# Optimization experiments

Hardware: AMD Instinct MI355X
Metric: run time of the kernel (lower is better)

The kernel has to match this reference:

```python
import jax, jax.numpy as jnp
import numpy as np

N = 100000   # nodes
E = 1200000  # edges
H = 64       # hidden_channels
G = 256      # graphs in the batch
C_IN = 1
C_OUT = 2


def setup_inputs() -> dict:
    key = jax.random.key(0)
    ks = jax.random.split(key, 16)

    def lin_w(k, fan_in, fan_out):
        bound = 1.0 / np.sqrt(fan_in)
        return jax.random.uniform(k, (fan_in, fan_out), jnp.float32, -bound, bound)

    def lin_b(k, fan_in, fan_out):
        bound = 1.0 / np.sqrt(fan_in)
        return jax.random.uniform(k, (fan_out,), jnp.float32, -bound, bound)

    return {
        "x": jax.random.normal(ks[0], (N, C_IN), jnp.float32),
        "edge_index": jax.random.randint(ks[1], (2, E), 0, N),
        "batch": jnp.sort(jax.random.randint(ks[2], (N,), 0, G)),
        "edge_weight": jax.random.uniform(ks[3], (E,), jnp.float32),
        # GraphConv 1: lin_rel (bias) + lin_root (no bias)
        "W1_rel": lin_w(ks[4], C_IN, H), "b1": lin_b(ks[5], C_IN, H), "W1_root": lin_w(ks[6], C_IN, H),
        # GraphConv 2
        "W2_rel": lin_w(ks[7], H, H), "b2": lin_b(ks[8], H, H), "W2_root": lin_w(ks[9], H, H),
        # GraphConv 3
        "W3_rel": lin_w(ks[10], H, H), "b3": lin_b(ks[11], H, H), "W3_root": lin_w(ks[12], H, H),
        # head
        "W_lin": lin_w(ks[13], H, C_OUT), "b_lin": lin_b(ks[14], H, C_OUT),
    }


def _graph_conv(x, src, dst, ew, W_rel, b_rel, W_root):
    # message: edge_weight * x[src]; aggr='add' to dst; then lin_rel(aggr) + lin_root(x)
    m = x[src] * ew[:, None]                                    # [E, C]
    agg = jax.ops.segment_sum(m, dst, num_segments=x.shape[0])  # [N, C]
    return agg @ W_rel + b_rel + x @ W_root


def reference(x, edge_index, batch, edge_weight,
              W1_rel, b1, W1_root, W2_rel, b2, W2_root, W3_rel, b3, W3_root,
              W_lin, b_lin):
    src, dst = edge_index[0], edge_index[1]
    h = jax.nn.relu(_graph_conv(x, src, dst, edge_weight, W1_rel, b1, W1_root))
    h = jax.nn.relu(_graph_conv(h, src, dst, edge_weight, W2_rel, b2, W2_root))
    h = _graph_conv(h, src, dst, edge_weight, W3_rel, b3, W3_root)
    # global mean pool over graph id
    sums = jax.ops.segment_sum(h, batch, num_segments=G)                        # [G, H]
    cnts = jax.ops.segment_sum(jnp.ones((h.shape[0],), h.dtype), batch, num_segments=G)
    pooled = sums / jnp.maximum(cnts, 1.0)[:, None]
    # dropout is identity in eval mode
    return pooled @ W_lin + b_lin                                               # [G, 2]
```

## Files before the change

### kernel.cpp

```cpp
#include <hip/hip_runtime.h>


#define BKT_SHIFT 7
#define BKT_SZ    128
#define NBK_MAX   1024
#define CHUNK     4096

static __device__ __forceinline__ float4 ld4(const float* p) {
    return *reinterpret_cast<const float4*>(p);
}
static __device__ __forceinline__ float rdlane(float v, int i) {
    return __int_as_float(__builtin_amdgcn_readlane(__float_as_int(v), i));
}

__global__ void k_small(const float* __restrict__ W3_rel, const float* __restrict__ b3,
                        const float* __restrict__ W3_root, const float* __restrict__ W_lin,
                        float4* __restrict__ MC4, float* __restrict__ b3W,
                        int* __restrict__ zbase, int zwords)
{
    int gt = blockIdx.x * 256 + threadIdx.x;
    for (int i = gt; i < zwords; i += gridDim.x * 256) zbase[i] = 0;

    if (blockIdx.x == 0) {
        int t = threadIdx.x;
        if (t < 64) {
            float sr0 = 0.f, sr1 = 0.f, so0 = 0.f, so1 = 0.f;
            for (int k = 0; k < 64; ++k) {
                float wl0 = W_lin[k * 2 + 0], wl1 = W_lin[k * 2 + 1];
                sr0 += W3_rel[t * 64 + k] * wl0;
                sr1 += W3_rel[t * 64 + k] * wl1;
                so0 += W3_root[t * 64 + k] * wl0;
                so1 += W3_root[t * 64 + k] * wl1;
            }
            MC4[t] = make_float4(sr0, sr1, so0, so1);
        }
        if (t < 2) {
            float s = 0.f;
            for (int k = 0; k < 64; ++k) s += b3[k] * W_lin[k * 2 + t];
            b3W[t] = s;
        }
    }
}

__global__ __launch_bounds__(256) void k_hist2(const int* __restrict__ dst,
                                               int* __restrict__ bcnt, int E, int NBK)
{
    __shared__ int lh[NBK_MAX];
    for (int i = threadIdx.x; i < NBK; i += 256) lh[i] = 0;
    __syncthreads();
    int e0 = blockIdx.x * CHUNK;
#pragma unroll
    for (int k = 0; k < 16; ++k) {
        int e = e0 + k * 256 + threadIdx.x;
        if (e < E) atomicAdd(&lh[dst[e] >> BKT_SHIFT], 1);
    }
    __syncthreads();
    for (int i = threadIdx.x; i < NBK; i += 256) {
        int v = lh[i];
        if (v) atomicAdd(&bcnt[i], v);
    }
}

__global__ __launch_bounds__(256) void k_scanb(const int* __restrict__ bcnt,
                                               int* __restrict__ bb, int NBK)
{
    __shared__ int tmp[256];
    int t = threadIdx.x;
    int loc[4]; int s = 0;
#pragma unroll
    for (int u = 0; u < 4; ++u) {
        int idx = t * 4 + u;
        loc[u] = (idx < NBK) ? bcnt[idx] : 0;
        s += loc[u];
    }
    tmp[t] = s;
    __syncthreads();
    for (int off = 1; off < 256; off <<= 1) {
        int v = (t >= off) ? tmp[t - off] : 0;
        __syncthreads();
        tmp[t] += v;
        __syncthreads();
    }
    int run = tmp[t] - s;
#pragma unroll
    for (int u = 0; u < 4; ++u) {
        int idx = t * 4 + u;
        if (idx < NBK) bb[idx] = run;
        run += loc[u];
    }
    if (t == 255) bb[NBK] = run;
}

__global__ __launch_bounds__(256) void k_scatter2(const int* __restrict__ src,
                                                  const int* __restrict__ dst,
                                                  const float* __restrict__ ew,
                                                  const int* __restrict__ bb,
                                                  int* __restrict__ cursor,
                                                  int2* __restrict__ ebuf, int E, int NBK)
{
    __shared__ int lofs[NBK_MAX + 1];
    __shared__ int rcur[NBK_MAX];
    __shared__ int delta[NBK_MAX];
    __shared__ int2 stage[CHUNK];
    __shared__ unsigned short sbkt[CHUNK];
    __shared__ int tmp[256];

    const int t = threadIdx.x;
    const int e0 = blockIdx.x * CHUNK;
    const int cnt = min(CHUNK, E - e0);

    for (int i = t; i < NBK; i += 256) lofs[i] = 0;
    __syncthreads();

    int   myb[16];
    int   mypk[16];
    float myw[16];
#pragma unroll
    for (int k = 0; k < 16; ++k) {
        int e = e0 + k * 256 + t;
        myb[k] = -1;
        if (e < E) {
            int d = dst[e];
            int b = d >> BKT_SHIFT;
            myb[k]  = b;
            mypk[k] = ((d & (BKT_SZ - 1)) << 17) | src[e];
            myw[k]  = ew[e];
            atomicAdd(&lofs[b], 1);
        }
    }
    __syncthreads();

    int loc[4]; int s = 0;
#pragma unroll
    for (int u = 0; u < 4; ++u) {
        int idx = t * 4 + u;
        loc[u] = (idx < NBK) ? lofs[idx] : 0;
        s += loc[u];
    }
    tmp[t] = s;
    __syncthreads();
    for (int off = 1; off < 256; off <<= 1) {
        int v = (t >= off) ? tmp[t - off] : 0;
        __syncthreads();
        tmp[t] += v;
        __syncthreads();
    }
    int run = tmp[t] - s;
#pragma unroll
    for (int u = 0; u < 4; ++u) {
        int idx = t * 4 + u;
        if (idx < NBK) { lofs[idx] = run; rcur[idx] = run; }
        run += loc[u];
    }
    if (t == 255) lofs[NBK] = run;
    __syncthreads();

    for (int b = t; b < NBK; b += 256) {
        int c = lofs[b + 1] - lofs[b];
        if (c > 0) {
            int g0 = atomicAdd(&cursor[b], c);
            delta[b] = bb[b] + g0 - lofs[b];
        }
    }
    __syncthreads();

#pragma unroll
    for (int k = 0; k < 16; ++k) {
        if (myb[k] >= 0) {
            int p = atomicAdd(&rcur[myb[k]], 1);
            stage[p] = make_int2(mypk[k], __float_as_int(myw[k]));
            sbkt[p]  = (unsigned short)myb[k];
        }
    }
    __syncthreads();

    for (int i = t; i < cnt; i += 256) {
        int b = sbkt[i];
        ebuf[delta[b] + i] = stage[i];
    }
}

__global__ __launch_bounds__(256) void k_sort3(const int2* __restrict__ ebuf,
                                               const int* __restrict__ bb,
                                               int* __restrict__ rowptr,
                                               int2* __restrict__ csr,
                                               int N, int E, int NBK)
{
    __shared__ int cnt_[BKT_SZ];
    __shared__ int sc[BKT_SZ];
    __shared__ int base_[BKT_SZ];
    __shared__ int cur_[BKT_SZ];

    const int t = threadIdx.x;
    const int bk = blockIdx.x;
    if (t < BKT_SZ) cnt_[t] = 0;
    __syncthreads();

    const int beg = bb[bk], end = bb[bk + 1];
    for (int i = beg + t; i < end; i += 256) {
        int dl = ebuf[i].x >> 17;
        atomicAdd(&cnt_[dl], 1);
    }
    __syncthreads();

    if (t < BKT_SZ) sc[t] = cnt_[t];
    __syncthreads();
    for (int off = 1; off < BKT_SZ; off <<= 1) {
        int v = (t < BKT_SZ && t >= off) ? sc[t - off] : 0;
        __syncthreads();
        if (t < BKT_SZ) sc[t] += v;
        __syncthreads();
    }
    if (t < BKT_SZ) {
        base_[t] = sc[t] - cnt_[t];
        cur_[t] = 0;
        int n = bk * BKT_SZ + t;
        if (n < N) rowptr[n] = beg + base_[t];
    }
    if (bk == 0 && t == 0) rowptr[N] = E;
    __syncthreads();

    for (int i = beg + t; i < end; i += 256) {
        int2 pw = ebuf[i];
        int dl = pw.x >> 17;
        int pos = beg + base_[dl] + atomicAdd(&cur_[dl], 1);
        csr[pos] = make_int2(pw.x & 0x1FFFF, pw.y);
    }
}

__global__ __launch_bounds__(256) void k_agg1(const int2* __restrict__ csr,
                                              const int* __restrict__ rowptr,
                                              const float* __restrict__ x,
                                              float2* __restrict__ axn, int N)
{
    int gt = blockIdx.x * 256 + threadIdx.x;
    int n = gt >> 2, p = gt & 3;
    if (n >= N) return;
    int b = rowptr[n], en = rowptr[n + 1];
    float a = 0.f;
    for (int e = b + p; e < en; e += 4) {
        int2 sw = csr[e];
        a = fmaf(__int_as_float(sw.y), x[sw.x], a);
    }
    a += __shfl_xor(a, 1);
    a += __shfl_xor(a, 2);
    if (p == 0) axn[n] = make_float2(a, x[n]);
}

__global__ __launch_bounds__(256) void k_agg2(const int2* __restrict__ csr,
                                              const int* __restrict__ rowptr,
                                              const float2* __restrict__ axn,
                                              const float* __restrict__ W1_rel,
                                              const float* __restrict__ b1,
                                              const float* __restrict__ W1_root,
                                              float* __restrict__ agg2, int N)
{
    int n = (blockIdx.x * 256 + threadIdx.x) >> 6;
    int lane = threadIdx.x & 63;
    if (n >= N) return;
    float wrel = W1_rel[lane], wroot = W1_root[lane], bj = b1[lane];
    int b = rowptr[n], en = rowptr[n + 1];
    float acc = 0.f;

    for (int base = b; base < en; base += 64) {
        int e = base + lane;
        float wv = 0.f;
        float2 ax = make_float2(0.f, 0.f);
        if (e < en) {
            int2 sw = csr[e];
            wv = __int_as_float(sw.y);
            ax = axn[sw.x];
        }
        int cnt = min(en - base, 64);
        int i = 0;
        for (; i + 4 <= cnt; i += 4) {
#pragma unroll
            for (int u = 0; u < 4; ++u) {
                float wi = rdlane(wv, i + u);
                float ai = rdlane(ax.x, i + u);
                float xi = rdlane(ax.y, i + u);
                float h = fmaxf(fmaf(ai, wrel, fmaf(xi, wroot, bj)), 0.f);
                acc = fmaf(wi, h, acc);
            }
        }
        for (; i < cnt; ++i) {
            float wi = rdlane(wv, i);
            float ai = rdlane(ax.x, i);
            float xi = rdlane(ax.y, i);
            float h = fmaxf(fmaf(ai, wrel, fmaf(xi, wroot, bj)), 0.f);
            acc = fmaf(wi, h, acc);
        }
    }
    agg2[(size_t)n * 64 + lane] = acc;
}

__global__ __launch_bounds__(256) void k_node2(const float* __restrict__ agg2,
                                               const float2* __restrict__ axn,
                                               const float* __restrict__ W2_rel,
                                               const float* __restrict__ W2_root,
                                               const float* __restrict__ b2,
                                               const float* __restrict__ W1_rel,
                                               const float* __restrict__ b1,
                                               const float* __restrict__ W1_root,
                                               const float* __restrict__ MCf,
                                               float2* __restrict__ z01,
                                               float2* __restrict__ z23, int N)
{
    __shared__ float As[128 * 65];

    const int t = threadIdx.x;
    const int n0 = blockIdx.x * 128;

#pragma unroll
    for (int it = 0; it < 8; ++it) {
        int idx = it * 256 + t;
        int nl = idx >> 4, q4 = (idx & 15) << 2;
        int n = n0 + nl;
        float4 a = (n < N) ? ld4(&agg2[(size_t)n * 64 + q4])
                           : make_float4(0.f, 0.f, 0.f, 0.f);
        float* row = &As[nl * 65 + q4];
        row[0] = a.x; row[1] = a.y; row[2] = a.z; row[3] = a.w;
    }
    __syncthreads();

    const int lane = t & 63;
    const int g = (t >> 7) & 1;
    const int hs = __builtin_amdgcn_readfirstlane((t >> 6) & 1);
    const int nl = g * 64 + lane;
    const int n = n0 + nl;
    float2 ax = (n < N) ? axn[n] : make_float2(0.f, 0.f);

    float4 acc[8];
#pragma unroll
    for (int q = 0; q < 8; ++q) acc[q] = make_float4(0.f, 0.f, 0.f, 0.f);

    const float* Asr = &As[nl * 65];

    for (int c = 0; c < 8; ++c) {
        float a_[8];
#pragma unroll
        for (int i = 0; i < 8; ++i) a_[i] = Asr[c * 8 + i];
#pragma unroll
        for (int i = 0; i < 8; ++i) {
            const float* wr = &W2_rel[(size_t)(c * 8 + i) * 64 + hs * 32];
#pragma unroll
            for (int q = 0; q < 8; ++q) {
                float4 w = ld4(wr + q * 4);
                acc[q].x = fmaf(a_[i], w.x, acc[q].x);
                acc[q].y = fmaf(a_[i], w.y, acc[q].y);
                acc[q].z = fmaf(a_[i], w.z, acc[q].z);
                acc[q].w = fmaf(a_[i], w.w, acc[q].w);
            }
        }
    }

    for (int c = 0; c < 8; ++c) {
        int k0 = c * 8;
        float4 w1ra = ld4(&W1_rel[k0]),  w1rb = ld4(&W1_rel[k0 + 4]);
        float4 w1oa = ld4(&W1_root[k0]), w1ob = ld4(&W1_root[k0 + 4]);
        float4 b1a  = ld4(&b1[k0]),      b1b  = ld4(&b1[k0 + 4]);
        float hk[8];
        hk[0] = fmaxf(fmaf(ax.x, w1ra.x, fmaf(ax.y, w1oa.x, b1a.x)), 0.f);
        hk[1] = fmaxf(fmaf(ax.x, w1ra.y, fmaf(ax.y, w1oa.y, b1a.y)), 0.f);
        hk[2] = fmaxf(fmaf(ax.x, w1ra.z, fmaf(ax.y, w1oa.z, b1a.z)), 0.f);
        hk[3] = fmaxf(fmaf(ax.x, w1ra.w, fmaf(ax.y, w1oa.w, b1a.w)), 0.f);
        hk[4] = fmaxf(fmaf(ax.x, w1rb.x, fmaf(ax.y, w1ob.x, b1b.x)), 0.f);
        hk[5] = fmaxf(fmaf(ax.x, w1rb.y, fmaf(ax.y, w1ob.y, b1b.y)), 0.f);
        hk[6] = fmaxf(fmaf(ax.x, w1rb.z, fmaf(ax.y, w1ob.z, b1b.z)), 0.f);
        hk[7] = fmaxf(fmaf(ax.x, w1rb.w, fmaf(ax.y, w1ob.w, b1b.w)), 0.f);
#pragma unroll
        for (int i = 0; i < 8; ++i) {
            const float* wo = &W2_root[(size_t)(k0 + i) * 64 + hs * 32];
#pragma unroll
            for (int q = 0; q < 8; ++q) {
                float4 w = ld4(wo + q * 4);
                acc[q].x = fmaf(hk[i], w.x, acc[q].x);
                acc[q].y = fmaf(hk[i], w.y, acc[q].y);
                acc[q].z = fmaf(hk[i], w.z, acc[q].z);
                acc[q].w = fmaf(hk[i], w.w, acc[q].w);
            }
        }
    }

    float z0 = 0.f, z1 = 0.f, z2 = 0.f, z3 = 0.f;
    const float* b2h = &b2[hs * 32];
#pragma unroll
    for (int q = 0; q < 8; ++q) {
        float4 bq = ld4(b2h + q * 4);
        int jb = hs * 32 + q * 4;
        float h2;
        h2 = fmaxf(acc[q].x + bq.x, 0.f);
        { const float* m = &MCf[(jb + 0) * 4];
          z0 = fmaf(h2, m[0], z0); z1 = fmaf(h2, m[1], z1);
          z2 = fmaf(h2, m[2], z2); z3 = fmaf(h2, m[3], z3); }
        h2 = fmaxf(acc[q].y + bq.y, 0.f);
        { const float* m = &MCf[(jb + 1) * 4];
          z0 = fmaf(h2, m[0], z0); z1 = fmaf(h2, m[1], z1);
          z2 = fmaf(h2, m[2], z2); z3 = fmaf(h2, m[3], z3); }
        h2 = fmaxf(acc[q].z + bq.z, 0.f);
        { const float* m = &MCf[(jb + 2) * 4];
          z0 = fmaf(h2, m[0], z0); z1 = fmaf(h2, m[1], z1);
          z2 = fmaf(h2, m[2], z2); z3 = fmaf(h2, m[3], z3); }
        h2 = fmaxf(acc[q].w + bq.w, 0.f);
        { const float* m = &MCf[(jb + 3) * 4];
          z0 = fmaf(h2, m[0], z0); z1 = fmaf(h2, m[1], z1);
          z2 = fmaf(h2, m[2], z2); z3 = fmaf(h2, m[3], z3); }
    }

    __syncthreads();
    float* zs = As;
    *reinterpret_cast<float4*>(&zs[(nl * 2 + hs) * 4]) = make_float4(z0, z1, z2, z3);
    __syncthreads();
    if (hs == 0 && n < N) {
        float4 p0 = *reinterpret_cast<float4*>(&zs[(nl * 2 + 0) * 4]);
        float4 p1 = *reinterpret_cast<float4*>(&zs[(nl * 2 + 1) * 4]);
        z01[n] = make_float2(p0.x + p1.x, p0.y + p1.y);
        z23[n] = make_float2(p0.z + p1.z, p0.w + p1.w);
    }
}

__global__ __launch_bounds__(256) void k_pool(const int2* __restrict__ csr,
                                              const int* __restrict__ rowptr,
                                              const int* __restrict__ batch,
                                              const float2* __restrict__ z01,
                                              const float2* __restrict__ z23,
                                              float* __restrict__ gacc, int N, int G)
{
    extern __shared__ float lds[];
    for (int i = threadIdx.x; i < 5 * G; i += 256) lds[i] = 0.f;
    __syncthreads();

    int gt = blockIdx.x * 256 + threadIdx.x;
    int n = gt >> 2, p = gt & 3;
    if (n < N) {
        int b = rowptr[n], en = rowptr[n + 1];
        float s0 = 0.f, s1 = 0.f;
        for (int e = b + p; e < en; e += 4) {
            int2 sw = csr[e];
            float w = __int_as_float(sw.y);
            float2 zz = z01[sw.x];
            s0 = fmaf(w, zz.x, s0);
            s1 = fmaf(w, zz.y, s1);
        }
        s0 += __shfl_xor(s0, 1);
        s0 += __shfl_xor(s0, 2);
        s1 += __shfl_xor(s1, 1);
        s1 += __shfl_xor(s1, 2);
        if (p == 0) {
            int bg = batch[n];
            float2 zw = z23[n];
            atomicAdd(&lds[bg * 5 + 0], s0);
            atomicAdd(&lds[bg * 5 + 1], s1);
            atomicAdd(&lds[bg * 5 + 2], zw.x);
            atomicAdd(&lds[bg * 5 + 3], zw.y);
            atomicAdd(&lds[bg * 5 + 4], 1.0f);
        }
    }
    __syncthreads();
    for (int i = threadIdx.x; i < 5 * G; i += 256) {
        float v = lds[i];
        if (v != 0.f) atomicAdd(&gacc[i], v);
    }
}

__global__ void k_final(const float* __restrict__ gacc, const float* __restrict__ b3W,
                        const float* __restrict__ b_lin, float* __restrict__ out, int G)
{
    int t = blockIdx.x * blockDim.x + threadIdx.x;
    if (t < G * 2) {
        int g = t >> 1, c = t & 1;
        float cnt = gacc[g * 5 + 4];
        float s = gacc[g * 5 + c] + gacc[g * 5 + 2 + c] + cnt * b3W[c];
        out[t] = s / fmaxf(cnt, 1.f) + b_lin[c];
    }
}

extern "C" void kernel_launch(void* const* d_in, const int* in_sizes, int n_in,
                              void* d_out, int out_size, void* d_ws, size_t ws_size,
                              hipStream_t stream)
{
    const float* x       = (const float*)d_in[0];
    const int*   ei      = (const int*)  d_in[1];
    const int*   batch   = (const int*)  d_in[2];
    const float* ew      = (const float*)d_in[3];
    const float* W1_rel  = (const float*)d_in[4];
    const float* b1      = (const float*)d_in[5];
    const float* W1_root = (const float*)d_in[6];
    const float* W2_rel  = (const float*)d_in[7];
    const float* b2      = (const float*)d_in[8];
    const float* W2_root = (const float*)d_in[9];
    const float* W3_rel  = (const float*)d_in[10];
    const float* b3      = (const float*)d_in[11];
    const float* W3_root = (const float*)d_in[12];
    const float* W_lin   = (const float*)d_in[13];
    const float* b_lin   = (const float*)d_in[14];
    float* out = (float*)d_out;

    const int N = in_sizes[0];
    const int E = in_sizes[3];
    const int G = out_size / 2;
    const int NBK = (N + BKT_SZ - 1) >> BKT_SHIFT;
    const int EB  = (E + CHUNK - 1) / CHUNK;
    const int* src = ei;
    const int* dst = ei + E;

    char* wsb = (char*)d_ws;
    size_t o = 0;
    auto take = [&](size_t bytes) -> char* {
        char* p = wsb + o;
        o += (bytes + 15) & ~(size_t)15;
        return p;
    };
    int*    cursor = (int*)   take((size_t)NBK * 4);
    int*    bcnt   = (int*)   take((size_t)NBK * 4);
    float*  gacc   = (float*) take((size_t)G * 5 * 4);
    size_t  zero_bytes = o;
    int*    bb     = (int*)   take((size_t)(NBK + 1) * 4);
    int*    rowptr = (int*)   take((size_t)(N + 1) * 4);
    int2*   ebuf   = (int2*)  take((size_t)E * 8);
    int2*   csr    = (int2*)  take((size_t)E * 8);
    float2* axn    = (float2*)take((size_t)N * 8);
    float*  agg2   = (float*) take((size_t)N * 64 * 4);
    float2* z01    = (float2*)take((size_t)N * 8);
    float2* z23    = (float2*)take((size_t)N * 8);
    float4* MC4    = (float4*)take(64 * 16);
    float*  b3W    = (float*) take(4 * 4);

    const int zwords = (int)(zero_bytes / 4);

    hipLaunchKernelGGL(k_small, dim3(8), dim3(256), 0, stream,
                       W3_rel, b3, W3_root, W_lin, MC4, b3W,
                       (int*)d_ws, zwords);

    hipLaunchKernelGGL(k_hist2, dim3(EB), dim3(256), 0, stream, dst, bcnt, E, NBK);
    hipLaunchKernelGGL(k_scanb, dim3(1), dim3(256), 0, stream, bcnt, bb, NBK);
    hipLaunchKernelGGL(k_scatter2, dim3(EB), dim3(256), 0, stream,
                       src, dst, ew, bb, cursor, ebuf, E, NBK);
    hipLaunchKernelGGL(k_sort3, dim3(NBK), dim3(256), 0, stream,
                       ebuf, bb, rowptr, csr, N, E, NBK);

    hipLaunchKernelGGL(k_agg1, dim3(((size_t)N * 4 + 255) / 256), dim3(256), 0, stream,
                       csr, rowptr, x, axn, N);

    hipLaunchKernelGGL(k_agg2, dim3((N * 64 + 255) / 256), dim3(256), 0, stream,
                       csr, rowptr, axn, W1_rel, b1, W1_root, agg2, N);

    hipLaunchKernelGGL(k_node2, dim3((N + 127) / 128), dim3(256), 0, stream,
                       agg2, axn, W2_rel, W2_root, b2, W1_rel, b1, W1_root,
                       (const float*)MC4, z01, z23, N);

    hipLaunchKernelGGL(k_pool, dim3(((size_t)N * 4 + 255) / 256), dim3(256),
                       5 * G * sizeof(float), stream,
                       csr, rowptr, batch, z01, z23, gacc, N, G);

    hipLaunchKernelGGL(k_final, dim3((G * 2 + 255) / 256), dim3(256), 0, stream,
                       gacc, b3W, b_lin, out, G);
}
```

Measured before the change: 143.8 us.

## Fuse layer-1 aggregation into CSR sort and layer-2 aggregation into node transform

Layer-1 scalar aggregation now happens inside the bucket sort kernel through LDS float atomics, which removes the separate k_agg1 pass. The layer-2 gather is fused into the node-transform kernel: each block aggregates its 128 nodes into shared memory, so the N×64 agg2 buffer never goes through global memory. The z23 pooling contributions are also accumulated inside that fused kernel, which drops the z23 buffer. The trade-off is fewer blocks (one per 128-node bucket) doing serial per-node gathers, so occupancy and load balance may suffer. Float atomics in LDS also make the summation order nondeterministic.

```diff
diff --git a/kernel.cpp b/kernel.cpp
--- a/kernel.cpp
+++ b/kernel.cpp
@@ -180,20 +180,23 @@
     }
 }
 
-__global__ __launch_bounds__(256) void k_sort3(const int2* __restrict__ ebuf,
-                                               const int* __restrict__ bb,
-                                               int* __restrict__ rowptr,
-                                               int2* __restrict__ csr,
-                                               int N, int E, int NBK)
+__global__ __launch_bounds__(256) void k_sort3a(const int2* __restrict__ ebuf,
+                                                const int* __restrict__ bb,
+                                                const float* __restrict__ x,
+                                                int* __restrict__ rowptr,
+                                                int2* __restrict__ csr,
+                                                float2* __restrict__ axn,
+                                                int N, int E)
 {
     __shared__ int cnt_[BKT_SZ];
     __shared__ int sc[BKT_SZ];
     __shared__ int base_[BKT_SZ];
     __shared__ int cur_[BKT_SZ];
+    __shared__ float a1[BKT_SZ];
 
     const int t = threadIdx.x;
     const int bk = blockIdx.x;
-    if (t < BKT_SZ) cnt_[t] = 0;
+    if (t < BKT_SZ) { cnt_[t] = 0; a1[t] = 0.f; }
     __syncthreads();
 
     const int beg = bb[bk], end = bb[bk + 1];
@@ -223,118 +226,88 @@
     for (int i = beg + t; i < end; i += 256) {
         int2 pw = ebuf[i];
         int dl = pw.x >> 17;
+        int s_ = pw.x & 0x1FFFF;
         int pos = beg + base_[dl] + atomicAdd(&cur_[dl], 1);
-        csr[pos] = make_int2(pw.x & 0x1FFFF, pw.y);
-    }
-}
-
-__global__ __launch_bounds__(256) void k_agg1(const int2* __restrict__ csr,
-                                              const int* __restrict__ rowptr,
-                                              const float* __restrict__ x,
-                                              float2* __restrict__ axn, int N)
-{
-    int gt = blockIdx.x * 256 + threadIdx.x;
-    int n = gt >> 2, p = gt & 3;
-    if (n >= N) return;
-    int b = rowptr[n], en = rowptr[n + 1];
-    float a = 0.f;
-    for (int e = b + p; e < en; e += 4) {
-        int2 sw = csr[e];
-        a = fmaf(__int_as_float(sw.y), x[sw.x], a);
-    }
-    a += __shfl_xor(a, 1);
-    a += __shfl_xor(a, 2);
-    if (p == 0) axn[n] = make_float2(a, x[n]);
-}
-
-__global__ __launch_bounds__(256) void k_agg2(const int2* __restrict__ csr,
-                                              const int* __restrict__ rowptr,
-                                              const float2* __restrict__ axn,
-                                              const float* __restrict__ W1_rel,
-                                              const float* __restrict__ b1,
-                                              const float* __restrict__ W1_root,
-                                              float* __restrict__ agg2, int N)
-{
-    int n = (blockIdx.x * 256 + threadIdx.x) >> 6;
-    int lane = threadIdx.x & 63;
-    if (n >= N) return;
-    float wrel = W1_rel[lane], wroot = W1_root[lane], bj = b1[lane];
-    int b = rowptr[n], en = rowptr[n + 1];
-    float acc = 0.f;
-
-    for (int base = b; base < en; base += 64) {
-        int e = base + lane;
-        float wv = 0.f;
-        float2 ax = make_float2(0.f, 0.f);
-        if (e < en) {
-            int2 sw = csr[e];
-            wv = __int_as_float(sw.y);
-            ax = axn[sw.x];
-        }
-        int cnt = min(en - base, 64);
-        int i = 0;
-        for (; i + 4 <= cnt; i += 4) {
-#pragma unroll
-            for (int u = 0; u < 4; ++u) {
-                float wi = rdlane(wv, i + u);
-                float ai = rdlane(ax.x, i + u);
-                float xi = rdlane(ax.y, i + u);
-                float h = fmaxf(fmaf(ai, wrel, fmaf(xi, wroot, bj)), 0.f);
-                acc = fmaf(wi, h, acc);
-            }
-        }
-        for (; i < cnt; ++i) {
-            float wi = rdlane(wv, i);
-            float ai = rdlane(ax.x, i);
-            float xi = rdlane(ax.y, i);
-            float h = fmaxf(fmaf(ai, wrel, fmaf(xi, wroot, bj)), 0.f);
-            acc = fmaf(wi, h, acc);
-        }
-    }
-    agg2[(size_t)n * 64 + lane] = acc;
-}
-
-__global__ __launch_bounds__(256) void k_node2(const float* __restrict__ agg2,
+        csr[pos] = make_int2(s_, pw.y);
+        atomicAdd(&a1[dl], __int_as_float(pw.y) * x[s_]);
+    }
+    __syncthreads();
+
+    int n = bk * BKT_SZ + t;
+    if (t < BKT_SZ && n < N) axn[n] = make_float2(a1[t], x[n]);
+}
+
+__global__ __launch_bounds__(256) void k_agg2n(const int2* __restrict__ csr,
+                                               const int* __restrict__ rowptr,
                                                const float2* __restrict__ axn,
+                                               const int* __restrict__ batch,
+                                               const float* __restrict__ W1_rel,
+                                               const float* __restrict__ b1,
+                                               const float* __restrict__ W1_root,
                                                const float* __restrict__ W2_rel,
                                                const float* __restrict__ W2_root,
                                                const float* __restrict__ b2,
-                                               const float* __restrict__ W1_rel,
-                                               const float* __restrict__ b1,
-                                               const float* __restrict__ W1_root,
                                                const float* __restrict__ MCf,
                                                float2* __restrict__ z01,
-                                               float2* __restrict__ z23, int N)
-{
-    __shared__ float As[128 * 65];
+                                               float* __restrict__ gacc,
+                                               int N, int G)
+{
+    __shared__ float T[BKT_SZ * 65];
+    __shared__ float bins[256 * 3];
 
     const int t = threadIdx.x;
-    const int n0 = blockIdx.x * 128;
-
-#pragma unroll
-    for (int it = 0; it < 8; ++it) {
-        int idx = it * 256 + t;
-        int nl = idx >> 4, q4 = (idx & 15) << 2;
-        int n = n0 + nl;
-        float4 a = (n < N) ? ld4(&agg2[(size_t)n * 64 + q4])
-                           : make_float4(0.f, 0.f, 0.f, 0.f);
-        float* row = &As[nl * 65 + q4];
-        row[0] = a.x; row[1] = a.y; row[2] = a.z; row[3] = a.w;
-    }
-    __syncthreads();
-
+    const int bk = blockIdx.x;
+    const int n0 = bk * BKT_SZ;
     const int lane = t & 63;
-    const int g = (t >> 7) & 1;
+    const int wave = t >> 6;
+
+    for (int i = t; i < 3 * G; i += 256) bins[i] = 0.f;
+
+    const float wrel = W1_rel[lane], wroot = W1_root[lane], bj = b1[lane];
+
+    int nn = n0 + wave * 32 + lane;
+    int rp = 0;
+    if (lane <= 32) rp = rowptr[min(nn, N)];
+
+    for (int i = 0; i < 32; ++i) {
+        int nl = wave * 32 + i;
+        int b  = __builtin_amdgcn_readlane(rp, i);
+        int en = __builtin_amdgcn_readlane(rp, i + 1);
+        float acc = 0.f;
+        for (int base = b; base < en; base += 64) {
+            int e = base + lane;
+            float wv = 0.f;
+            float2 ax = make_float2(0.f, 0.f);
+            if (e < en) {
+                int2 sw = csr[e];
+                wv = __int_as_float(sw.y);
+                ax = axn[sw.x];
+            }
+            int cntm = min(en - base, 64);
+#pragma unroll 4
+            for (int j = 0; j < cntm; ++j) {
+                float wj = rdlane(wv, j);
+                float aj = rdlane(ax.x, j);
+                float xj = rdlane(ax.y, j);
+                float h = fmaxf(fmaf(aj, wrel, fmaf(xj, wroot, bj)), 0.f);
+                acc = fmaf(wj, h, acc);
+            }
+        }
+        T[nl * 65 + lane] = acc;
+    }
+    __syncthreads();
+
+    const int g  = (t >> 7) & 1;
     const int hs = __builtin_amdgcn_readfirstlane((t >> 6) & 1);
     const int nl = g * 64 + lane;
-    const int n = n0 + nl;
+    const int n  = n0 + nl;
     float2 ax = (n < N) ? axn[n] : make_float2(0.f, 0.f);
 
     float4 acc[8];
 #pragma unroll
     for (int q = 0; q < 8; ++q) acc[q] = make_float4(0.f, 0.f, 0.f, 0.f);
 
-    const float* Asr = &As[nl * 65];
+    const float* Asr = &T[nl * 65];
 
     for (int c = 0; c < 8; ++c) {
         float a_[8];
@@ -408,26 +381,36 @@
     }
 
     __syncthreads();
-    float* zs = As;
+    float* zs = T;
     *reinterpret_cast<float4*>(&zs[(nl * 2 + hs) * 4]) = make_float4(z0, z1, z2, z3);
     __syncthreads();
     if (hs == 0 && n < N) {
         float4 p0 = *reinterpret_cast<float4*>(&zs[(nl * 2 + 0) * 4]);
         float4 p1 = *reinterpret_cast<float4*>(&zs[(nl * 2 + 1) * 4]);
         z01[n] = make_float2(p0.x + p1.x, p0.y + p1.y);
-        z23[n] = make_float2(p0.z + p1.z, p0.w + p1.w);
-    }
-}
-
-__global__ __launch_bounds__(256) void k_pool(const int2* __restrict__ csr,
-                                              const int* __restrict__ rowptr,
-                                              const int* __restrict__ batch,
-                                              const float2* __restrict__ z01,
-                                              const float2* __restrict__ z23,
-                                              float* __restrict__ gacc, int N, int G)
-{
-    extern __shared__ float lds[];
-    for (int i = threadIdx.x; i < 5 * G; i += 256) lds[i] = 0.f;
+        int bg = batch[n];
+        atomicAdd(&bins[bg * 3 + 0], p0.z + p1.z);
+        atomicAdd(&bins[bg * 3 + 1], p0.w + p1.w);
+        atomicAdd(&bins[bg * 3 + 2], 1.0f);
+    }
+    __syncthreads();
+    for (int i = t; i < 3 * G; i += 256) {
+        float v = bins[i];
+        if (v != 0.f) {
+            int gg = i / 3, c = i % 3;
+            atomicAdd(&gacc[gg * 5 + 2 + c], v);
+        }
+    }
+}
+
+__global__ __launch_bounds__(256) void k_poole(const int2* __restrict__ csr,
+                                               const int* __restrict__ rowptr,
+                                               const int* __restrict__ batch,
+                                               const float2* __restrict__ z01,
+                                               float* __restrict__ gacc, int N, int G)
+{
+    __shared__ float lds[2 * 256];
+    for (int i = threadIdx.x; i < 2 * G; i += 256) lds[i] = 0.f;
     __syncthreads();
 
     int gt = blockIdx.x * 256 + threadIdx.x;
@@ -448,18 +431,14 @@
         s1 += __shfl_xor(s1, 2);
         if (p == 0) {
             int bg = batch[n];
-            float2 zw = z23[n];
-            atomicAdd(&lds[bg * 5 + 0], s0);
-            atomicAdd(&lds[bg * 5 + 1], s1);
-            atomicAdd(&lds[bg * 5 + 2], zw.x);
-            atomicAdd(&lds[bg * 5 + 3], zw.y);
-            atomicAdd(&lds[bg * 5 + 4], 1.0f);
-        }
-    }
-    __syncthreads();
-    for (int i = threadIdx.x; i < 5 * G; i += 256) {
+            atomicAdd(&lds[bg * 2 + 0], s0);
+            atomicAdd(&lds[bg * 2 + 1], s1);
+        }
+    }
+    __syncthreads();
+    for (int i = threadIdx.x; i < 2 * G; i += 256) {
         float v = lds[i];
-        if (v != 0.f) atomicAdd(&gacc[i], v);
+        if (v != 0.f) atomicAdd(&gacc[(i >> 1) * 5 + (i & 1)], v);
     }
 }
 
@@ -520,9 +499,7 @@
     int2*   ebuf   = (int2*)  take((size_t)E * 8);
     int2*   csr    = (int2*)  take((size_t)E * 8);
     float2* axn    = (float2*)take((size_t)N * 8);
-    float*  agg2   = (float*) take((size_t)N * 64 * 4);
     float2* z01    = (float2*)take((size_t)N * 8);
-    float2* z23    = (float2*)take((size_t)N * 8);
     float4* MC4    = (float4*)take(64 * 16);
     float*  b3W    = (float*) take(4 * 4);
 
@@ -536,22 +513,16 @@
     hipLaunchKernelGGL(k_scanb, dim3(1), dim3(256), 0, stream, bcnt, bb, NBK);
     hipLaunchKernelGGL(k_scatter2, dim3(EB), dim3(256), 0, stream,
                        src, dst, ew, bb, cursor, ebuf, E, NBK);
-    hipLaunchKernelGGL(k_sort3, dim3(NBK), dim3(256), 0, stream,
-                       ebuf, bb, rowptr, csr, N, E, NBK);
-
-    hipLaunchKernelGGL(k_agg1, dim3(((size_t)N * 4 + 255) / 256), dim3(256), 0, stream,
-                       csr, rowptr, x, axn, N);
-
-    hipLaunchKernelGGL(k_agg2, dim3((N * 64 + 255) / 256), dim3(256), 0, stream,
-                       csr, rowptr, axn, W1_rel, b1, W1_root, agg2, N);
-
-    hipLaunchKernelGGL(k_node2, dim3((N + 127) / 128), dim3(256), 0, stream,
-                       agg2, axn, W2_rel, W2_root, b2, W1_rel, b1, W1_root,
-                       (const float*)MC4, z01, z23, N);
-
-    hipLaunchKernelGGL(k_pool, dim3(((size_t)N * 4 + 255) / 256), dim3(256),
-                       5 * G * sizeof(float), stream,
-                       csr, rowptr, batch, z01, z23, gacc, N, G);
+    hipLaunchKernelGGL(k_sort3a, dim3(NBK), dim3(256), 0, stream,
+                       ebuf, bb, x, rowptr, csr, axn, N, E);
+
+    hipLaunchKernelGGL(k_agg2n, dim3(NBK), dim3(256), 0, stream,
+                       csr, rowptr, axn, batch, W1_rel, b1, W1_root,
+                       W2_rel, W2_root, b2, (const float*)MC4,
+                       z01, gacc, N, G);
+
+    hipLaunchKernelGGL(k_poole, dim3(((size_t)N * 4 + 255) / 256), dim3(256), 0, stream,
+                       csr, rowptr, batch, z01, gacc, N, G);
 
     hipLaunchKernelGGL(k_final, dim3((G * 2 + 255) / 256), dim3(256), 0, stream,
                        gacc, b3W, b_lin, out, G);
```

Result: slower. 147.0 us (median of 2 runs) (+2.3%).

## Use fixed-capacity edge buckets and fuse first-layer aggregation into the bucket sort

Applied to the files above, without the earlier changes.

Removes the destination histogram and scan kernels by giving each 128-node bucket a fixed CAP-sized slot in the edge buffer; the scatter cursor then doubles as the bucket count. The first-layer scalar aggregation is folded into the per-bucket sort kernel using LDS float atomics, which removes the separate k_agg1 pass. Row pointers become begin/end int2 pairs, and the k_agg2 broadcast loop is unrolled by 8 with padding. The cost is that nothing handles a bucket overflowing CAP, so correctness depends on the input degree distribution; the LDS atomics also make the summation order non-deterministic, and the pool kernel now assumes G is at most 256.

```diff
diff --git a/kernel.cpp b/kernel.cpp
--- a/kernel.cpp
+++ b/kernel.cpp
@@ -5,6 +5,7 @@
 #define BKT_SZ    128
 #define NBK_MAX   1024
 #define CHUNK     4096
+#define CAP       2048
 
 static __device__ __forceinline__ float4 ld4(const float* p) {
     return *reinterpret_cast<const float4*>(p);
@@ -42,59 +43,9 @@
     }
 }
 
-__global__ __launch_bounds__(256) void k_hist2(const int* __restrict__ dst,
-                                               int* __restrict__ bcnt, int E, int NBK)
-{
-    __shared__ int lh[NBK_MAX];
-    for (int i = threadIdx.x; i < NBK; i += 256) lh[i] = 0;
-    __syncthreads();
-    int e0 = blockIdx.x * CHUNK;
-#pragma unroll
-    for (int k = 0; k < 16; ++k) {
-        int e = e0 + k * 256 + threadIdx.x;
-        if (e < E) atomicAdd(&lh[dst[e] >> BKT_SHIFT], 1);
-    }
-    __syncthreads();
-    for (int i = threadIdx.x; i < NBK; i += 256) {
-        int v = lh[i];
-        if (v) atomicAdd(&bcnt[i], v);
-    }
-}
-
-__global__ __launch_bounds__(256) void k_scanb(const int* __restrict__ bcnt,
-                                               int* __restrict__ bb, int NBK)
-{
-    __shared__ int tmp[256];
-    int t = threadIdx.x;
-    int loc[4]; int s = 0;
-#pragma unroll
-    for (int u = 0; u < 4; ++u) {
-        int idx = t * 4 + u;
-        loc[u] = (idx < NBK) ? bcnt[idx] : 0;
-        s += loc[u];
-    }
-    tmp[t] = s;
-    __syncthreads();
-    for (int off = 1; off < 256; off <<= 1) {
-        int v = (t >= off) ? tmp[t - off] : 0;
-        __syncthreads();
-        tmp[t] += v;
-        __syncthreads();
-    }
-    int run = tmp[t] - s;
-#pragma unroll
-    for (int u = 0; u < 4; ++u) {
-        int idx = t * 4 + u;
-        if (idx < NBK) bb[idx] = run;
-        run += loc[u];
-    }
-    if (t == 255) bb[NBK] = run;
-}
-
 __global__ __launch_bounds__(256) void k_scatter2(const int* __restrict__ src,
                                                   const int* __restrict__ dst,
                                                   const float* __restrict__ ew,
-                                                  const int* __restrict__ bb,
                                                   int* __restrict__ cursor,
                                                   int2* __restrict__ ebuf, int E, int NBK)
 {
@@ -159,7 +110,7 @@
         int c = lofs[b + 1] - lofs[b];
         if (c > 0) {
             int g0 = atomicAdd(&cursor[b], c);
-            delta[b] = bb[b] + g0 - lofs[b];
+            delta[b] = b * CAP + g0 - lofs[b];
         }
     }
     __syncthreads();
@@ -180,23 +131,26 @@
     }
 }
 
-__global__ __launch_bounds__(256) void k_sort3(const int2* __restrict__ ebuf,
-                                               const int* __restrict__ bb,
-                                               int* __restrict__ rowptr,
-                                               int2* __restrict__ csr,
-                                               int N, int E, int NBK)
+__global__ __launch_bounds__(256) void k_sort3a(const int2* __restrict__ ebuf,
+                                                const int* __restrict__ bcnt,
+                                                const float* __restrict__ x,
+                                                int2* __restrict__ rowptr2,
+                                                int2* __restrict__ csr,
+                                                float2* __restrict__ axn, int N)
 {
     __shared__ int cnt_[BKT_SZ];
     __shared__ int sc[BKT_SZ];
     __shared__ int base_[BKT_SZ];
     __shared__ int cur_[BKT_SZ];
+    __shared__ float a1[BKT_SZ];
 
     const int t = threadIdx.x;
     const int bk = blockIdx.x;
-    if (t < BKT_SZ) cnt_[t] = 0;
-    __syncthreads();
-
-    const int beg = bb[bk], end = bb[bk + 1];
+    if (t < BKT_SZ) { cnt_[t] = 0; a1[t] = 0.f; }
+    __syncthreads();
+
+    const int beg = bk * CAP;
+    const int end = beg + bcnt[bk];
     for (int i = beg + t; i < end; i += 256) {
         int dl = ebuf[i].x >> 17;
         atomicAdd(&cnt_[dl], 1);
@@ -215,40 +169,26 @@
         base_[t] = sc[t] - cnt_[t];
         cur_[t] = 0;
         int n = bk * BKT_SZ + t;
-        if (n < N) rowptr[n] = beg + base_[t];
-    }
-    if (bk == 0 && t == 0) rowptr[N] = E;
+        if (n < N) rowptr2[n] = make_int2(beg + base_[t], beg + base_[t] + cnt_[t]);
+    }
     __syncthreads();
 
     for (int i = beg + t; i < end; i += 256) {
         int2 pw = ebuf[i];
         int dl = pw.x >> 17;
+        int s_ = pw.x & 0x1FFFF;
         int pos = beg + base_[dl] + atomicAdd(&cur_[dl], 1);
-        csr[pos] = make_int2(pw.x & 0x1FFFF, pw.y);
-    }
-}
-
-__global__ __launch_bounds__(256) void k_agg1(const int2* __restrict__ csr,
-                                              const int* __restrict__ rowptr,
-                                              const float* __restrict__ x,
-                                              float2* __restrict__ axn, int N)
-{
-    int gt = blockIdx.x * 256 + threadIdx.x;
-    int n = gt >> 2, p = gt & 3;
-    if (n >= N) return;
-    int b = rowptr[n], en = rowptr[n + 1];
-    float a = 0.f;
-    for (int e = b + p; e < en; e += 4) {
-        int2 sw = csr[e];
-        a = fmaf(__int_as_float(sw.y), x[sw.x], a);
-    }
-    a += __shfl_xor(a, 1);
-    a += __shfl_xor(a, 2);
-    if (p == 0) axn[n] = make_float2(a, x[n]);
+        csr[pos] = make_int2(pw.x, pw.y);
+        atomicAdd(&a1[dl], __int_as_float(pw.y) * x[s_]);
+    }
+    __syncthreads();
+
+    int n = bk * BKT_SZ + t;
+    if (t < BKT_SZ && n < N) axn[n] = make_float2(a1[t], x[n]);
 }
 
 __global__ __launch_bounds__(256) void k_agg2(const int2* __restrict__ csr,
-                                              const int* __restrict__ rowptr,
+                                              const int2* __restrict__ rowptr2,
                                               const float2* __restrict__ axn,
                                               const float* __restrict__ W1_rel,
                                               const float* __restrict__ b1,
@@ -259,36 +199,28 @@
     int lane = threadIdx.x & 63;
     if (n >= N) return;
     float wrel = W1_rel[lane], wroot = W1_root[lane], bj = b1[lane];
-    int b = rowptr[n], en = rowptr[n + 1];
+    int2 rp = rowptr2[n];
     float acc = 0.f;
 
-    for (int base = b; base < en; base += 64) {
+    for (int base = rp.x; base < rp.y; base += 64) {
         int e = base + lane;
         float wv = 0.f;
         float2 ax = make_float2(0.f, 0.f);
-        if (e < en) {
+        if (e < rp.y) {
             int2 sw = csr[e];
             wv = __int_as_float(sw.y);
-            ax = axn[sw.x];
-        }
-        int cnt = min(en - base, 64);
-        int i = 0;
-        for (; i + 4 <= cnt; i += 4) {
-#pragma unroll
-            for (int u = 0; u < 4; ++u) {
+            ax = axn[sw.x & 0x1FFFF];
+        }
+        int m8 = (min(rp.y - base, 64) + 7) & ~7;
+        for (int i = 0; i < m8; i += 8) {
+#pragma unroll
+            for (int u = 0; u < 8; ++u) {
                 float wi = rdlane(wv, i + u);
                 float ai = rdlane(ax.x, i + u);
                 float xi = rdlane(ax.y, i + u);
                 float h = fmaxf(fmaf(ai, wrel, fmaf(xi, wroot, bj)), 0.f);
                 acc = fmaf(wi, h, acc);
             }
-        }
-        for (; i < cnt; ++i) {
-            float wi = rdlane(wv, i);
-            float ai = rdlane(ax.x, i);
-            float xi = rdlane(ax.y, i);
-            float h = fmaxf(fmaf(ai, wrel, fmaf(xi, wroot, bj)), 0.f);
-            acc = fmaf(wi, h, acc);
         }
     }
     agg2[(size_t)n * 64 + lane] = acc;
@@ -420,25 +352,25 @@
 }
 
 __global__ __launch_bounds__(256) void k_pool(const int2* __restrict__ csr,
-                                              const int* __restrict__ rowptr,
+                                              const int2* __restrict__ rowptr2,
                                               const int* __restrict__ batch,
                                               const float2* __restrict__ z01,
                                               const float2* __restrict__ z23,
                                               float* __restrict__ gacc, int N, int G)
 {
-    extern __shared__ float lds[];
+    __shared__ float lds[5 * 256];
     for (int i = threadIdx.x; i < 5 * G; i += 256) lds[i] = 0.f;
     __syncthreads();
 
     int gt = blockIdx.x * 256 + threadIdx.x;
     int n = gt >> 2, p = gt & 3;
     if (n < N) {
-        int b = rowptr[n], en = rowptr[n + 1];
+        int2 rp = rowptr2[n];
         float s0 = 0.f, s1 = 0.f;
-        for (int e = b + p; e < en; e += 4) {
+        for (int e = rp.x + p; e < rp.y; e += 4) {
             int2 sw = csr[e];
             float w = __int_as_float(sw.y);
-            float2 zz = z01[sw.x];
+            float2 zz = z01[sw.x & 0x1FFFF];
             s0 = fmaf(w, zz.x, s0);
             s1 = fmaf(w, zz.y, s1);
         }
@@ -511,20 +443,18 @@
         o += (bytes + 15) & ~(size_t)15;
         return p;
     };
-    int*    cursor = (int*)   take((size_t)NBK * 4);
-    int*    bcnt   = (int*)   take((size_t)NBK * 4);
-    float*  gacc   = (float*) take((size_t)G * 5 * 4);
+    int*    cursor  = (int*)   take((size_t)NBK * 4);
+    float*  gacc    = (float*) take((size_t)G * 5 * 4);
     size_t  zero_bytes = o;
-    int*    bb     = (int*)   take((size_t)(NBK + 1) * 4);
-    int*    rowptr = (int*)   take((size_t)(N + 1) * 4);
-    int2*   ebuf   = (int2*)  take((size_t)E * 8);
-    int2*   csr    = (int2*)  take((size_t)E * 8);
-    float2* axn    = (float2*)take((size_t)N * 8);
-    float*  agg2   = (float*) take((size_t)N * 64 * 4);
-    float2* z01    = (float2*)take((size_t)N * 8);
-    float2* z23    = (float2*)take((size_t)N * 8);
-    float4* MC4    = (float4*)take(64 * 16);
-    float*  b3W    = (float*) take(4 * 4);
+    int2*   rowptr2 = (int2*)  take((size_t)N * 8);
+    int2*   ebuf    = (int2*)  take((size_t)NBK * CAP * 8);
+    int2*   csr     = (int2*)  take((size_t)NBK * CAP * 8);
+    float2* axn     = (float2*)take((size_t)N * 8);
+    float*  agg2    = (float*) take((size_t)N * 64 * 4);
+    float2* z01     = (float2*)take((size_t)N * 8);
+    float2* z23     = (float2*)take((size_t)N * 8);
+    float4* MC4     = (float4*)take(64 * 16);
+    float*  b3W     = (float*) take(4 * 4);
 
     const int zwords = (int)(zero_bytes / 4);
 
@@ -532,26 +462,21 @@
                        W3_rel, b3, W3_root, W_lin, MC4, b3W,
                        (int*)d_ws, zwords);
 
-    hipLaunchKernelGGL(k_hist2, dim3(EB), dim3(256), 0, stream, dst, bcnt, E, NBK);
-    hipLaunchKernelGGL(k_scanb, dim3(1), dim3(256), 0, stream, bcnt, bb, NBK);
     hipLaunchKernelGGL(k_scatter2, dim3(EB), dim3(256), 0, stream,
-                       src, dst, ew, bb, cursor, ebuf, E, NBK);
-    hipLaunchKernelGGL(k_sort3, dim3(NBK), dim3(256), 0, stream,
-                       ebuf, bb, rowptr, csr, N, E, NBK);
-
-    hipLaunchKernelGGL(k_agg1, dim3(((size_t)N * 4 + 255) / 256), dim3(256), 0, stream,
-                       csr, rowptr, x, axn, N);
+                       src, dst, ew, cursor, ebuf, E, NBK);
+
+    hipLaunchKernelGGL(k_sort3a, dim3(NBK), dim3(256), 0, stream,
+                       ebuf, cursor, x, rowptr2, csr, axn, N);
 
     hipLaunchKernelGGL(k_agg2, dim3((N * 64 + 255) / 256), dim3(256), 0, stream,
-                       csr, rowptr, axn, W1_rel, b1, W1_root, agg2, N);
+                       csr, rowptr2, axn, W1_rel, b1, W1_root, agg2, N);
 
     hipLaunchKernelGGL(k_node2, dim3((N + 127) / 128), dim3(256), 0, stream,
                        agg2, axn, W2_rel, W2_root, b2, W1_rel, b1, W1_root,
                        (const float*)MC4, z01, z23, N);
 
-    hipLaunchKernelGGL(k_pool, dim3(((size_t)N * 4 + 255) / 256), dim3(256),
-                       5 * G * sizeof(float), stream,
-                       csr, rowptr, batch, z01, z23, gacc, N, G);
+    hipLaunchKernelGGL(k_pool, dim3(((size_t)N * 4 + 255) / 256), dim3(256), 0, stream,
+                       csr, rowptr2, batch, z01, z23, gacc, N, G);
 
     hipLaunchKernelGGL(k_final, dim3((G * 2 + 255) / 256), dim3(256), 0, stream,
                        gacc, b3W, b_lin, out, G);
```

New measurement: 125.1 us. 13.0% less time.
